# Kernel tuning notes

Hardware: AMD Instinct MI355X
Metric: run time of the kernel (lower is better)

Reference implementation:

```python
import jax, jax.numpy as jnp
import numpy as np

SIGMAS = (0.02, 0.01, 0.008)   # self.sig
SIGMA_N = 0.5                  # self.sig_n
COORD_SCALE = 0.05             # keep distances commensurate with sigmas


def setup_inputs() -> dict:
    key = jax.random.key(0)
    k1, k2, k3 = jax.random.split(key, 3)
    B, Vn, Fn = 2, 5000, 6144
    predictions = jax.random.uniform(k1, (B, Vn, 3), dtype=jnp.float32) * COORD_SCALE
    targets = jax.random.uniform(k2, (B, Vn, 3), dtype=jnp.float32) * COORD_SCALE
    faces = jax.random.randint(k3, (Fn, 3), 0, Vn, dtype=jnp.int32)
    return {"predictions": predictions, "targets": targets, "faces": faces}


def _mesh_quantities(V, F):
    # face centers C [F,3], areas L [F,1], unit normals Nn [F,3]
    v0, v1, v2 = V[F[:, 0]], V[F[:, 1]], V[F[:, 2]]
    C = (v0 + v1 + v2) / 3.0
    N = 0.5 * jnp.cross(v1 - v0, v2 - v0)
    L = jnp.sqrt((N * N).sum(-1, keepdims=True) + 1e-24)
    return C, L, N / L


def _varifold_prod(C1, L1, N1, C2, L2, N2, sigma, sigma_n):
    # <mu1, mu2> = sum_ij L1_i L2_j exp(-|c_i-c_j|^2/sigma^2) exp((<n_i,n_j>-1)/sigma_n^2)
    d2 = ((C1[:, None, :] - C2[None, :, :]) ** 2).sum(-1)          # [F,F]
    ndot = N1 @ N2.T                                               # [F,F]
    K = jnp.exp(-d2 / (sigma * sigma) + (ndot - 1.0) / (sigma_n * sigma_n))
    return (L1[:, 0] * (K @ L2[:, 0])).sum()


def reference(predictions, targets, faces):
    def per_sample(Vs, Vt):
        Cs, Ls, Ns = _mesh_quantities(Vs, faces)
        Ct, Lt, Nt = _mesh_quantities(Vt, faces)
        li = jnp.float32(0.0)
        for sig in SIGMAS:  # small fixed set of sigmas
            w = (sig / SIGMAS[0]) ** 2
            pss = _varifold_prod(Cs, Ls, Ns, Cs, Ls, Ns, sig, SIGMA_N)
            pst = _varifold_prod(Cs, Ls, Ns, Ct, Lt, Nt, sig, SIGMA_N)
            ptt = _varifold_prod(Ct, Lt, Nt, Ct, Lt, Nt, sig, SIGMA_N)
            li = li + w * (pss - 2.0 * pst + ptt)
        return li

    L = jax.vmap(per_sample)(predictions, targets)  # [B]
    return jnp.mean(L)
```

## Files before the change

### kernel.cpp

```cpp
#include <hip/hip_runtime.h>

#define F_FACES 6144
#define VN      5000
#define BATCH   2

#define SC_F    30.02806022f
#define SN_F    2.40224481f
#define C4_F    5.7707801635558535f

__device__ __forceinline__ float fast_exp2(float x) {
    float r;
    asm("v_exp_f32 %0, %1" : "=v"(r) : "v"(x));
    return r;
}

__global__ __launch_bounds__(256) void mesh_prep(
    const float* __restrict__ pred, const float* __restrict__ targ,
    const int* __restrict__ faces, float4* __restrict__ ws4,
    float* __restrict__ out)
{
    const int f = blockIdx.x * 256 + threadIdx.x;
    const int m = blockIdx.y;
    if (blockIdx.x == 0 && m == 0 && threadIdx.x == 0) out[0] = 0.0f;
    if (f >= F_FACES) return;

    const int b = m >> 1, which = m & 1;
    const float* V = (which ? targ : pred) + b * (VN * 3);

    const int i0 = faces[3 * f + 0];
    const int i1 = faces[3 * f + 1];
    const int i2 = faces[3 * f + 2];

    const float v0x = V[3 * i0 + 0], v0y = V[3 * i0 + 1], v0z = V[3 * i0 + 2];
    const float v1x = V[3 * i1 + 0], v1y = V[3 * i1 + 1], v1z = V[3 * i1 + 2];
    const float v2x = V[3 * i2 + 0], v2y = V[3 * i2 + 1], v2z = V[3 * i2 + 2];

    const float Cx = (v0x + v1x + v2x) * (1.0f / 3.0f);
    const float Cy = (v0y + v1y + v2y) * (1.0f / 3.0f);
    const float Cz = (v0z + v1z + v2z) * (1.0f / 3.0f);

    const float e1x = v1x - v0x, e1y = v1y - v0y, e1z = v1z - v0z;
    const float e2x = v2x - v0x, e2y = v2y - v0y, e2z = v2z - v0z;

    const float Nx = 0.5f * (e1y * e2z - e1z * e2y);
    const float Ny = 0.5f * (e1z * e2x - e1x * e2z);
    const float Nz = 0.5f * (e1x * e2y - e1y * e2x);

    const float l2  = Nx * Nx + Ny * Ny + Nz * Nz + 1e-24f;
    const float L   = sqrtf(l2);
    const float inv = 1.0f / L;

    const float Csx = Cx * SC_F, Csy = Cy * SC_F, Csz = Cz * SC_F;
    const float a   = -(Csx * Csx + Csy * Csy + Csz * Csz);
    const float s   = inv * SN_F;

    const long base = (long)(m * F_FACES + f) * 2;
    ws4[base + 0] = make_float4(Csx, Csy, Csz, a);
    ws4[base + 1] = make_float4(Nx * s, Ny * s, Nz * s, log2f(L) - C4_F);
}

#define IT        4
#define TJ        64
#define BLK       128
#define J_CHUNKS  (F_FACES / TJ)
#define I_ROWS    (BLK * IT)
#define I_TILES   (F_FACES / I_ROWS)
#define N_ST      (I_TILES * J_CHUNKS)
#define N_TRI     624
#define N_BLOCKS  (2 * N_ST + 4 * N_TRI)

__global__ __launch_bounds__(BLK) void varifold_pairs(
    const float4* __restrict__ ws4, float* __restrict__ out)
{
    __shared__ float4 sAB[2 * TJ];
    __shared__ float  red[2];

    const int tid = threadIdx.x;

    int c, b, it, jc;
    {
        const int bi = blockIdx.x;
        if (bi < 2 * N_ST) {
            c = 1; b = bi / N_ST;
            const int lin = bi % N_ST;
            it = lin / J_CHUNKS; jc = lin % J_CHUNKS;
        } else {
            const int r = bi - 2 * N_ST;
            const int q = r / N_TRI;
            c = (q & 2) ? 2 : 0; b = q & 1;
            int lin = r - q * N_TRI;
            it = 0;
            int w = J_CHUNKS;
            while (lin >= w) { lin -= w; ++it; w -= 8; }
            jc = 8 * it + lin;
        }
    }

    const int m1 = b * 2 + (c == 2 ? 1 : 0);
    const int m2 = b * 2 + (c >= 1 ? 1 : 0);
    const int iBase = it * I_ROWS;
    const int jBase = jc * TJ;

    const bool straddle = (c != 1) && (jc < 8 * (it + 1));
    const float wOut = (c == 1) ? -1.0f : (straddle ? 0.5f : 1.0f);

    const float4* P1 = ws4 + (long)m1 * (F_FACES * 2);
    const float4* P2 = ws4 + (long)m2 * (F_FACES * 2);

    float C2x[IT], C2y[IT], C2z[IT], Ai[IT];
    float Nix[IT], Niy[IT], Niz[IT], Li[IT];
    float acc[IT];
    int   iIdx[IT];

#pragma unroll
    for (int k = 0; k < IT; ++k) {
        const int i = iBase + k * BLK + tid;
        iIdx[k] = i;
        const float4 A  = P1[2 * i + 0];
        const float4 Bv = P1[2 * i + 1];
        C2x[k] = 2.0f * A.x; C2y[k] = 2.0f * A.y; C2z[k] = 2.0f * A.z;
        Ai[k]  = A.w;
        Nix[k] = Bv.x; Niy[k] = Bv.y; Niz[k] = Bv.z;
        Li[k]  = fast_exp2(Bv.w + C4_F);
        acc[k] = 0.0f;
    }

    sAB[tid] = P2[2 * jBase + tid];
    __syncthreads();

    if (!straddle) {
#pragma unroll 4
        for (int jj = 0; jj < TJ; ++jj) {
            const float4 a4 = sAB[2 * jj + 0];
            const float4 b4 = sAB[2 * jj + 1];
#pragma unroll
            for (int k = 0; k < IT; ++k) {
                float r = fmaf(C2x[k], a4.x, a4.w);
                r = fmaf(C2y[k], a4.y, r);
                r = fmaf(C2z[k], a4.z, r);
                const float t0 = fast_exp2(r + Ai[k]);
                float n = fmaf(Nix[k], b4.x, b4.w);
                n = fmaf(Niy[k], b4.y, n);
                n = fmaf(Niz[k], b4.z, n);
                const float en = fast_exp2(n);
                const float t2  = t0 * t0;
                const float t4  = t2 * t2;
                const float t8  = t4 * t4;
                const float t16 = t8 * t8;
                const float t24 = t16 * t8;
                const float t25 = t24 * t0;
                float p = fmaf(0.25f, t16, t4);
                p = fmaf(0.16f, t25, p);
                acc[k] = fmaf(en, p, acc[k]);
            }
        }
    } else {
#pragma unroll 4
        for (int jj = 0; jj < TJ; ++jj) {
            const float4 a4 = sAB[2 * jj + 0];
            const float4 b4 = sAB[2 * jj + 1];
            const int j = jBase + jj;
#pragma unroll
            for (int k = 0; k < IT; ++k) {
                float r = fmaf(C2x[k], a4.x, a4.w);
                r = fmaf(C2y[k], a4.y, r);
                r = fmaf(C2z[k], a4.z, r);
                const float t0 = fast_exp2(r + Ai[k]);
                float n = fmaf(Nix[k], b4.x, b4.w);
                n = fmaf(Niy[k], b4.y, n);
                n = fmaf(Niz[k], b4.z, n);
                const float en = fast_exp2(n);
                const float t2  = t0 * t0;
                const float t4  = t2 * t2;
                const float t8  = t4 * t4;
                const float t16 = t8 * t8;
                const float t24 = t16 * t8;
                const float t25 = t24 * t0;
                float p = fmaf(0.25f, t16, t4);
                p = fmaf(0.16f, t25, p);
                float f = (j > iIdx[k]) ? 2.0f : 0.0f;
                f = (j == iIdx[k]) ? 1.0f : f;
                acc[k] = fmaf(f * en, p, acc[k]);
            }
        }
    }

    float part = 0.0f;
#pragma unroll
    for (int k = 0; k < IT; ++k) part = fmaf(acc[k], Li[k], part);

#pragma unroll
    for (int off = 32; off; off >>= 1) part += __shfl_xor(part, off);
    if ((tid & 63) == 0) red[tid >> 6] = part;
    __syncthreads();
    if (tid == 0) atomicAdd(out, wOut * (red[0] + red[1]));
}

extern "C" void kernel_launch(void* const* d_in, const int* in_sizes, int n_in,
                              void* d_out, int out_size, void* d_ws, size_t ws_size,
                              hipStream_t stream) {
    const float* pred  = (const float*)d_in[0];
    const float* targ  = (const float*)d_in[1];
    const int*   faces = (const int*)d_in[2];
    float*       out   = (float*)d_out;
    float4*      ws4   = (float4*)d_ws;

    dim3 g1(F_FACES / 256, 2 * BATCH);
    mesh_prep<<<g1, 256, 0, stream>>>(pred, targ, faces, ws4, out);

    varifold_pairs<<<dim3(N_BLOCKS), dim3(BLK), 0, stream>>>(ws4, out);
}
```

Before: 136.1 us.

## Balance pair work with flat column partitioning and spread atomics over cells

Replaces the per-tile block mapping with a flat enumeration of all j-columns across the triangular and full bands. Each block handles exactly 25 columns and may cross band boundaries, reloading its i-row registers only when the band changes. Atomics go to 64 padded cells instead of one address, and a small finalize kernel sums the cells. The goal is even load per block and less atomic contention. The cost is tiny 25-column segments with a barrier per segment, a non-unrolled inner loop and an extra kernel launch.

Result: faster. 130.2 us (-4.3%).

```diff
diff --git a/kernel.cpp b/kernel.cpp
--- a/kernel.cpp
+++ b/kernel.cpp
@@ -2,7 +2,6 @@
 
 #define F_FACES 6144
 #define VN      5000
-#define BATCH   2
 
 #define SC_F    30.02806022f
 #define SN_F    2.40224481f
@@ -14,14 +13,17 @@
     return r;
 }
 
+#define CELLS_OFF_FLOATS (4 * F_FACES * 2 * 4)
+
 __global__ __launch_bounds__(256) void mesh_prep(
     const float* __restrict__ pred, const float* __restrict__ targ,
     const int* __restrict__ faces, float4* __restrict__ ws4,
-    float* __restrict__ out)
+    float* __restrict__ cells)
 {
     const int f = blockIdx.x * 256 + threadIdx.x;
     const int m = blockIdx.y;
-    if (blockIdx.x == 0 && m == 0 && threadIdx.x == 0) out[0] = 0.0f;
+    if (blockIdx.x == 0 && m == 0 && threadIdx.x < 64)
+        cells[threadIdx.x * 16] = 0.0f;
     if (f >= F_FACES) return;
 
     const int b = m >> 1, which = m & 1;
@@ -59,141 +61,162 @@
     ws4[base + 1] = make_float4(Nx * s, Ny * s, Nz * s, log2f(L) - C4_F);
 }
 
+#define BLK       128
 #define IT        4
-#define TJ        64
-#define BLK       128
-#define J_CHUNKS  (F_FACES / TJ)
 #define I_ROWS    (BLK * IT)
 #define I_TILES   (F_FACES / I_ROWS)
-#define N_ST      (I_TILES * J_CHUNKS)
-#define N_TRI     624
-#define N_BLOCKS  (2 * N_ST + 4 * N_TRI)
-
-__global__ __launch_bounds__(BLK) void varifold_pairs(
-    const float4* __restrict__ ws4, float* __restrict__ out)
+#define W_TRI_Q   39936
+#define TRI_TOTAL (4 * W_TRI_Q)
+#define TOTAL_COLS 307200
+#define N_BLOCKS  12288
+#define CPB       25
+
+__global__ __launch_bounds__(BLK, 8) void varifold_pairs(
+    const float4* __restrict__ ws4, float* __restrict__ cells)
 {
-    __shared__ float4 sAB[2 * TJ];
+    __shared__ float4 sAB[2 * CPB];
     __shared__ float  red[2];
 
     const int tid = threadIdx.x;
-
-    int c, b, it, jc;
-    {
-        const int bi = blockIdx.x;
-        if (bi < 2 * N_ST) {
-            c = 1; b = bi / N_ST;
-            const int lin = bi % N_ST;
-            it = lin / J_CHUNKS; jc = lin % J_CHUNKS;
-        } else {
-            const int r = bi - 2 * N_ST;
-            const int q = r / N_TRI;
-            c = (q & 2) ? 2 : 0; b = q & 1;
-            int lin = r - q * N_TRI;
-            it = 0;
-            int w = J_CHUNKS;
-            while (lin >= w) { lin -= w; ++it; w -= 8; }
-            jc = 8 * it + lin;
-        }
-    }
-
-    const int m1 = b * 2 + (c == 2 ? 1 : 0);
-    const int m2 = b * 2 + (c >= 1 ? 1 : 0);
-    const int iBase = it * I_ROWS;
-    const int jBase = jc * TJ;
-
-    const bool straddle = (c != 1) && (jc < 8 * (it + 1));
-    const float wOut = (c == 1) ? -1.0f : (straddle ? 0.5f : 1.0f);
-
-    const float4* P1 = ws4 + (long)m1 * (F_FACES * 2);
-    const float4* P2 = ws4 + (long)m2 * (F_FACES * 2);
-
+    int col = blockIdx.x * CPB;
+    int remaining = CPB;
+    float total = 0.0f;
+
+    int cur_key = -1;
     float C2x[IT], C2y[IT], C2z[IT], Ai[IT];
     float Nix[IT], Niy[IT], Niz[IT], Li[IT];
     float acc[IT];
-    int   iIdx[IT];
-
-#pragma unroll
-    for (int k = 0; k < IT; ++k) {
-        const int i = iBase + k * BLK + tid;
-        iIdx[k] = i;
-        const float4 A  = P1[2 * i + 0];
-        const float4 Bv = P1[2 * i + 1];
-        C2x[k] = 2.0f * A.x; C2y[k] = 2.0f * A.y; C2z[k] = 2.0f * A.z;
-        Ai[k]  = A.w;
-        Nix[k] = Bv.x; Niy[k] = Bv.y; Niz[k] = Bv.z;
-        Li[k]  = fast_exp2(Bv.w + C4_F);
-        acc[k] = 0.0f;
-    }
-
-    sAB[tid] = P2[2 * jBase + tid];
-    __syncthreads();
-
-    if (!straddle) {
-#pragma unroll 4
-        for (int jj = 0; jj < TJ; ++jj) {
-            const float4 a4 = sAB[2 * jj + 0];
-            const float4 b4 = sAB[2 * jj + 1];
+
+    while (remaining > 0) {
+        int c, b, it, j, r, bandLeft;
+        if (col < TRI_TOTAL) {
+            const int q = col / W_TRI_Q;
+            r = col - q * W_TRI_Q;
+            c = (q >> 1) ? 2 : 0; b = q & 1;
+            it = 0;
+            int w = F_FACES;
+            while (r >= w) { r -= w; ++it; w -= I_ROWS; }
+            j = it * I_ROWS + r;
+            bandLeft = w - r;
+        } else {
+            const int lin = col - TRI_TOTAL;
+            const int band = lin / F_FACES;
+            r = lin - band * F_FACES;
+            j = r;
+            b = band / I_TILES; it = band - (band / I_TILES) * I_TILES;
+            c = 1;
+            bandLeft = F_FACES - r;
+        }
+        const bool strad = (c != 1) && (r < I_ROWS);
+        int segLen = min(remaining, bandLeft);
+        if (strad) segLen = min(segLen, I_ROWS - r);
+        const float wOut = (c == 1) ? -1.0f : (strad ? 0.5f : 1.0f);
+        const int m1 = 2 * b + (c == 2 ? 1 : 0);
+        const int m2 = 2 * b + (c >= 1 ? 1 : 0);
+        const float4* P1 = ws4 + (long)m1 * (F_FACES * 2);
+        const float4* P2 = ws4 + (long)m2 * (F_FACES * 2);
+        const int iBase = it * I_ROWS;
+
+        const int key = m1 * 16 + it;
+        if (key != cur_key) {
+            cur_key = key;
 #pragma unroll
             for (int k = 0; k < IT; ++k) {
-                float r = fmaf(C2x[k], a4.x, a4.w);
-                r = fmaf(C2y[k], a4.y, r);
-                r = fmaf(C2z[k], a4.z, r);
-                const float t0 = fast_exp2(r + Ai[k]);
-                float n = fmaf(Nix[k], b4.x, b4.w);
-                n = fmaf(Niy[k], b4.y, n);
-                n = fmaf(Niz[k], b4.z, n);
-                const float en = fast_exp2(n);
-                const float t2  = t0 * t0;
-                const float t4  = t2 * t2;
-                const float t8  = t4 * t4;
-                const float t16 = t8 * t8;
-                const float t24 = t16 * t8;
-                const float t25 = t24 * t0;
-                float p = fmaf(0.25f, t16, t4);
-                p = fmaf(0.16f, t25, p);
-                acc[k] = fmaf(en, p, acc[k]);
+                const int i = iBase + k * BLK + tid;
+                const float4 A  = P1[2 * i + 0];
+                const float4 Bv = P1[2 * i + 1];
+                C2x[k] = 2.0f * A.x; C2y[k] = 2.0f * A.y; C2z[k] = 2.0f * A.z;
+                Ai[k]  = A.w;
+                Nix[k] = Bv.x; Niy[k] = Bv.y; Niz[k] = Bv.z;
+                Li[k]  = fast_exp2(Bv.w + C4_F);
             }
         }
-    } else {
-#pragma unroll 4
-        for (int jj = 0; jj < TJ; ++jj) {
-            const float4 a4 = sAB[2 * jj + 0];
-            const float4 b4 = sAB[2 * jj + 1];
-            const int j = jBase + jj;
-#pragma unroll
-            for (int k = 0; k < IT; ++k) {
-                float r = fmaf(C2x[k], a4.x, a4.w);
-                r = fmaf(C2y[k], a4.y, r);
-                r = fmaf(C2z[k], a4.z, r);
-                const float t0 = fast_exp2(r + Ai[k]);
-                float n = fmaf(Nix[k], b4.x, b4.w);
-                n = fmaf(Niy[k], b4.y, n);
-                n = fmaf(Niz[k], b4.z, n);
-                const float en = fast_exp2(n);
-                const float t2  = t0 * t0;
-                const float t4  = t2 * t2;
-                const float t8  = t4 * t4;
-                const float t16 = t8 * t8;
-                const float t24 = t16 * t8;
-                const float t25 = t24 * t0;
-                float p = fmaf(0.25f, t16, t4);
-                p = fmaf(0.16f, t25, p);
-                float f = (j > iIdx[k]) ? 2.0f : 0.0f;
-                f = (j == iIdx[k]) ? 1.0f : f;
-                acc[k] = fmaf(f * en, p, acc[k]);
+#pragma unroll
+        for (int k = 0; k < IT; ++k) acc[k] = 0.0f;
+
+        __syncthreads();
+        if (tid < 2 * segLen) sAB[tid] = P2[2 * j + tid];
+        __syncthreads();
+
+        if (!strad) {
+            for (int jj = 0; jj < segLen; ++jj) {
+                const float4 a4 = sAB[2 * jj + 0];
+                const float4 b4 = sAB[2 * jj + 1];
+#pragma unroll
+                for (int k = 0; k < IT; ++k) {
+                    float rr = fmaf(C2x[k], a4.x, a4.w);
+                    rr = fmaf(C2y[k], a4.y, rr);
+                    rr = fmaf(C2z[k], a4.z, rr);
+                    const float t0 = fast_exp2(rr + Ai[k]);
+                    float n = fmaf(Nix[k], b4.x, b4.w);
+                    n = fmaf(Niy[k], b4.y, n);
+                    n = fmaf(Niz[k], b4.z, n);
+                    const float en = fast_exp2(n);
+                    const float t2  = t0 * t0;
+                    const float t4  = t2 * t2;
+                    const float t8  = t4 * t4;
+                    const float t16 = t8 * t8;
+                    const float t24 = t16 * t8;
+                    const float t25 = t24 * t0;
+                    float p = fmaf(0.25f, t16, t4);
+                    p = fmaf(0.16f, t25, p);
+                    acc[k] = fmaf(en, p, acc[k]);
+                }
+            }
+        } else {
+            for (int jj = 0; jj < segLen; ++jj) {
+                const float4 a4 = sAB[2 * jj + 0];
+                const float4 b4 = sAB[2 * jj + 1];
+                const int jg = j + jj;
+#pragma unroll
+                for (int k = 0; k < IT; ++k) {
+                    const int i = iBase + k * BLK + tid;
+                    float rr = fmaf(C2x[k], a4.x, a4.w);
+                    rr = fmaf(C2y[k], a4.y, rr);
+                    rr = fmaf(C2z[k], a4.z, rr);
+                    const float t0 = fast_exp2(rr + Ai[k]);
+                    float n = fmaf(Nix[k], b4.x, b4.w);
+                    n = fmaf(Niy[k], b4.y, n);
+                    n = fmaf(Niz[k], b4.z, n);
+                    const float en = fast_exp2(n);
+                    const float t2  = t0 * t0;
+                    const float t4  = t2 * t2;
+                    const float t8  = t4 * t4;
+                    const float t16 = t8 * t8;
+                    const float t24 = t16 * t8;
+                    const float t25 = t24 * t0;
+                    float p = fmaf(0.25f, t16, t4);
+                    p = fmaf(0.16f, t25, p);
+                    float fw = (jg > i) ? 2.0f : 0.0f;
+                    fw = (jg == i) ? 1.0f : fw;
+                    acc[k] = fmaf(fw * en, p, acc[k]);
+                }
             }
         }
+
+        float part = 0.0f;
+#pragma unroll
+        for (int k = 0; k < IT; ++k) part = fmaf(acc[k], Li[k], part);
+        total = fmaf(wOut, part, total);
+
+        col += segLen; remaining -= segLen;
     }
 
-    float part = 0.0f;
-#pragma unroll
-    for (int k = 0; k < IT; ++k) part = fmaf(acc[k], Li[k], part);
-
-#pragma unroll
-    for (int off = 32; off; off >>= 1) part += __shfl_xor(part, off);
-    if ((tid & 63) == 0) red[tid >> 6] = part;
+#pragma unroll
+    for (int off = 32; off; off >>= 1) total += __shfl_xor(total, off);
+    if ((tid & 63) == 0) red[tid >> 6] = total;
     __syncthreads();
-    if (tid == 0) atomicAdd(out, wOut * (red[0] + red[1]));
+    if (tid == 0)
+        atomicAdd(&cells[(blockIdx.x & 63) * 16], red[0] + red[1]);
+}
+
+__global__ __launch_bounds__(64) void finalize_sum(
+    const float* __restrict__ cells, float* __restrict__ out)
+{
+    float v = cells[threadIdx.x * 16];
+#pragma unroll
+    for (int off = 32; off; off >>= 1) v += __shfl_xor(v, off);
+    if (threadIdx.x == 0) out[0] = v;
 }
 
 extern "C" void kernel_launch(void* const* d_in, const int* in_sizes, int n_in,
@@ -204,9 +227,12 @@
     const int*   faces = (const int*)d_in[2];
     float*       out   = (float*)d_out;
     float4*      ws4   = (float4*)d_ws;
-
-    dim3 g1(F_FACES / 256, 2 * BATCH);
-    mesh_prep<<<g1, 256, 0, stream>>>(pred, targ, faces, ws4, out);
-
-    varifold_pairs<<<dim3(N_BLOCKS), dim3(BLK), 0, stream>>>(ws4, out);
-}
+    float*       cells = (float*)d_ws + CELLS_OFF_FLOATS;
+
+    dim3 g1(F_FACES / 256, 4);
+    mesh_prep<<<g1, 256, 0, stream>>>(pred, targ, faces, ws4, cells);
+
+    varifold_pairs<<<dim3(N_BLOCKS), dim3(BLK), 0, stream>>>(ws4, cells);
+
+    finalize_sum<<<dim3(1), dim3(64), 0, stream>>>(cells, out);
+}
```
